# Kernel optimization log

Measured on AMD Instinct MI355X. Metric: run time of the kernel, lower is better.

## Reference

```python
import jax, jax.numpy as jnp
import numpy as np

SIG_EPS = 0.1
IN_DIM = 256
OUT_DIM = 64


def setup_inputs() -> dict:
    key = jax.random.key(0)
    ks = jax.random.split(key, 6)
    B, S, Q = 32, 512, 512
    return {
        "phi_support": jax.random.normal(ks[0], (B, S, IN_DIM), jnp.float32),
        "y_support": jax.random.normal(ks[1], (B, S, OUT_DIM), jnp.float32),
        "phi_query": jax.random.normal(ks[2], (B, Q, IN_DIM), jnp.float32),
        "y_query": jax.random.normal(ks[3], (B, Q, OUT_DIM), jnp.float32),
        # learned parameters (K init'd to zeros in torch, use small randn for a non-trivial test)
        "K": jax.random.normal(ks[4], (IN_DIM, OUT_DIM), jnp.float32) * 0.02,
        "L_asym": jax.random.normal(ks[5], (IN_DIM, IN_DIM), jnp.float32) * 0.1,
    }


def reference(phi_support, y_support, phi_query, y_query, K, L_asym):
    sig_eps = jnp.float32(SIG_EPS)
    log_sig_eps = jnp.log(sig_eps)
    out_dim = K.shape[1]

    L = L_asym @ L_asym.T  # [I, I]
    # nobs > 0 branch (n_support = 512)
    posterior_L = jnp.einsum('bsi,bsj->bij', phi_support, phi_support) + L[None]  # [B,I,I]
    posterior_L_inv = jnp.linalg.inv(posterior_L)
    rhs = jnp.einsum('bsi,bso->bio', phi_support, y_support) + (L @ K)[None]  # [B,I,O]
    posterior_K = posterior_L_inv @ rhs  # [B,I,O]

    mu_pred = phi_query @ posterior_K  # [B,Q,O]
    # spread_fac = 1 + diag quadratic form phi Linv phi^T  -> [B,Q]
    spread_fac = 1.0 + jnp.einsum('bqi,bij,bqj->bq', phi_query, posterior_L_inv, phi_query)
    eye_eps = jnp.eye(out_dim, dtype=phi_query.dtype) * sig_eps
    sig_pred = spread_fac[..., None, None] * eye_eps  # [B,Q,O,O]

    # predictive_nll: inverse of sig_pred is an exactly scaled identity, so the
    # quadratic form y^T inv(sig_pred) y == ||y||^2 / (spread_fac * sig_eps) (same math)
    diff = y_query - mu_pred
    quadf = jnp.sum(diff * diff, axis=-1) / (spread_fac * sig_eps)  # [B,Q]
    logdet = out_dim * (jnp.log(spread_fac) + log_sig_eps)  # [B,Q]
    predictive_nll = logdet.mean() + quadf.mean()

    return (mu_pred, sig_pred, predictive_nll)
```

## Files before the change

### kernel.cpp

```cpp
#include <hip/hip_runtime.h>
#include <hip/hip_cooperative_groups.h>
#include <math.h>

namespace cg = cooperative_groups;

#define B 32
#define S 512
#define Q 512
#define I 256
#define O 64
#define SIG_EPS 0.1f
#define LOG_SIG_EPS (-2.3025850929940457f)

#define WS_L 0
#define WS_T1 65536
#define WS_LKT 81920
#define WS_M0 98304
#define WS_M1 2195456
#define WS_RHST 4292608
#define WS_D 4816896
#define WS_U16 5079040
#define U_PTH 0
#define U_PTL 4194304
#define U_YTH 8388608
#define U_YTL 9437184
#define U_IVH 10485760
#define U_IVL 12582912
#define U_PKH 14680064
#define U_PKL 15204352

#define OUT_MU_ELEMS (B * Q * O)
#define OUT_SIG_ELEMS (B * Q * O * O)
#define OUT_NLL_IDX (OUT_MU_ELEMS + OUT_SIG_ELEMS)

typedef short short8 __attribute__((ext_vector_type(8)));
typedef float f32x4 __attribute__((ext_vector_type(4)));
#define MFMA16(a, b, c) __builtin_amdgcn_mfma_f32_16x16x32_bf16(a, b, c, 0, 0, 0)

struct Params {
  const float *phi_s, *y_s, *phi_q, *y_q, *Km, *La;
  float *Lm, *T1, *LKT, *M0, *M1, *RHST, *Dbuf;
  unsigned short *PTh, *PTl, *YTh, *YTl, *IVh, *IVl, *PKh, *PKl;
  float *mu, *nll;
  float4 *sig;
};

__device__ __forceinline__ f32x4 mfma3(short8 ah, short8 al, short8 bh, short8 bl, f32x4 c) {
  c = MFMA16(ah, bh, c);
  c = MFMA16(ah, bl, c);
  c = MFMA16(al, bh, c);
  return c;
}

__device__ __forceinline__ unsigned short f2bf(float x) {
  unsigned int u = __float_as_uint(x);
  return (unsigned short)((u + 0x7fffu + ((u >> 16) & 1u)) >> 16);
}
__device__ __forceinline__ float bf2f(unsigned short h) { return __uint_as_float(((unsigned int)h) << 16); }
__device__ __forceinline__ void split2(float x, unsigned short& h, unsigned short& l) {
  h = f2bf(x);
  l = f2bf(x - bf2f(h));
}
__device__ __forceinline__ void split4(float4 v, uint2& H, uint2& L) {
  unsigned short h0, h1, h2, h3, l0, l1, l2, l3;
  split2(v.x, h0, l0); split2(v.y, h1, l1); split2(v.z, h2, l2); split2(v.w, h3, l3);
  H.x = (unsigned)h0 | ((unsigned)h1 << 16); H.y = (unsigned)h2 | ((unsigned)h3 << 16);
  L.x = (unsigned)l0 | ((unsigned)l1 << 16); L.y = (unsigned)l2 | ((unsigned)l3 << 16);
}
__device__ __forceinline__ void cvt8(const float* p, short8& h8, short8& l8) {
  float4 a = *(const float4*)p;
  float4 b = *(const float4*)(p + 4);
  uint2 H0, L0, H1, L1;
  split4(a, H0, L0); split4(b, H1, L1);
  union { uint2 q[2]; short8 s; } uh, ul;
  uh.q[0] = H0; uh.q[1] = H1; ul.q[0] = L0; ul.q[1] = L1;
  h8 = uh.s; l8 = ul.s;
}
__device__ __forceinline__ short8 ld8(const unsigned short* p) { return *(const short8*)(const void*)p; }

__device__ __forceinline__ void fma4x4(const float4 av, const float4 bv, float acc[4][4]) {
  const float ar[4] = {av.x, av.y, av.z, av.w};
  const float br[4] = {bv.x, bv.y, bv.z, bv.w};
#pragma unroll
  for (int i = 0; i < 4; ++i)
#pragma unroll
    for (int j = 0; j < 4; ++j) acc[i][j] += ar[i] * br[j];
}

__device__ __forceinline__ void load_direct64(float* dst, int ds, const float* src, int ss, int t) {
#pragma unroll
  for (int m = 0; m < 4; ++m) {
    int r = (t >> 4) + 16 * m, c4 = (t & 15) * 4;
    *(float4*)&dst[r * ds + c4] = *(const float4*)&src[(size_t)r * ss + c4];
  }
}
__device__ __forceinline__ void load_trans64(float* dst, int ds, const float* src, int ss, int t) {
#pragma unroll
  for (int m = 0; m < 4; ++m) {
    int r = (t >> 4) + 16 * m, c4 = (t & 15) * 4;
    float4 v = *(const float4*)&src[(size_t)r * ss + c4];
    dst[(c4 + 0) * ds + r] = v.x;
    dst[(c4 + 1) * ds + r] = v.y;
    dst[(c4 + 2) * ds + r] = v.z;
    dst[(c4 + 3) * ds + r] = v.w;
  }
}
template <int SA, int SB>
__device__ __forceinline__ void gemm64(const float* At, const float* Bs, int tr, int tc, float acc[4][4]) {
#pragma unroll 8
  for (int kk = 0; kk < 64; ++kk) {
    float4 a = *(const float4*)&At[kk * SA + tr * 4];
    float4 b = *(const float4*)&Bs[kk * SB + tc * 4];
    fma4x4(a, b, acc);
  }
}

#define SC4(V) V.x *= pivinv; V.y *= pivinv; V.z *= pivinv; V.w *= pivinv
#define UP4(V, R) V.x -= g * R.x; V.y -= g * R.y; V.z -= g * R.z; V.w -= g * R.w

template <int TS>
__device__ void gj64(const float* T, float* rowbuf, float* Dout, int t) {
  int r = t >> 2, q = t & 3;
  int lane = t & 63;
  float4 A0 = *(const float4*)&T[r * TS + q * 16 + 0];
  float4 A1 = *(const float4*)&T[r * TS + q * 16 + 4];
  float4 A2 = *(const float4*)&T[r * TS + q * 16 + 8];
  float4 A3 = *(const float4*)&T[r * TS + q * 16 + 12];
#define IC(c) (((q * 16 + (c)) == r) ? 1.f : 0.f)
  float4 I0 = make_float4(IC(0), IC(1), IC(2), IC(3));
  float4 I1 = make_float4(IC(4), IC(5), IC(6), IC(7));
  float4 I2 = make_float4(IC(8), IC(9), IC(10), IC(11));
  float4 I3 = make_float4(IC(12), IC(13), IC(14), IC(15));
#undef IC
  for (int p = 0; p < 64; ++p) {
    float* RA = rowbuf + (p & 1) * 128;
    float* RI = RA + 64;
    if (r == p) {
      ((float4*)&RA[q * 16])[0] = A0; ((float4*)&RA[q * 16])[1] = A1;
      ((float4*)&RA[q * 16])[2] = A2; ((float4*)&RA[q * 16])[3] = A3;
      ((float4*)&RI[q * 16])[0] = I0; ((float4*)&RI[q * 16])[1] = I1;
      ((float4*)&RI[q * 16])[2] = I2; ((float4*)&RI[q * 16])[3] = I3;
    }
    __syncthreads();
    float pivinv = 1.0f / RA[p];
    int sidx = p & 15;
    float4 blk = (sidx < 8) ? ((sidx < 4) ? A0 : A1) : ((sidx < 12) ? A2 : A3);
    int sc = sidx & 3;
    float ap = (sc == 0) ? blk.x : (sc == 1) ? blk.y : (sc == 2) ? blk.z : blk.w;
    float f = __shfl(ap, (lane & ~3) | (p >> 4), 64);
    float4 ra0 = ((const float4*)&RA[q * 16])[0], ra1 = ((const float4*)&RA[q * 16])[1];
    float4 ra2 = ((const float4*)&RA[q * 16])[2], ra3 = ((const float4*)&RA[q * 16])[3];
    float4 ri0 = ((const float4*)&RI[q * 16])[0], ri1 = ((const float4*)&RI[q * 16])[1];
    float4 ri2 = ((const float4*)&RI[q * 16])[2], ri3 = ((const float4*)&RI[q * 16])[3];
    if (r == p) {
      SC4(A0); SC4(A1); SC4(A2); SC4(A3);
      SC4(I0); SC4(I1); SC4(I2); SC4(I3);
    } else {
      float g = f * pivinv;
      UP4(A0, ra0); UP4(A1, ra1); UP4(A2, ra2); UP4(A3, ra3);
      UP4(I0, ri0); UP4(I1, ri1); UP4(I2, ri2); UP4(I3, ri3);
    }
  }
  ((float4*)&Dout[r * 64 + q * 16])[0] = I0;
  ((float4*)&Dout[r * 64 + q * 16])[1] = I1;
  ((float4*)&Dout[r * 64 + q * 16])[2] = I2;
  ((float4*)&Dout[r * 64 + q * 16])[3] = I3;
}

__device__ void phase0_unit(const Params& p, int w, int t, float* smem) {
  if (w < 1280) {
    unsigned short* Hs = (unsigned short*)smem;
    unsigned short* Lo = Hs + 64 * 68;
    const float* src;
    unsigned short *dh, *dl;
    int sstride;
    if (w < 1024) {
      int b = w >> 5, r = w & 31, ic = r >> 3, sc = r & 7;
      src = p.phi_s + ((size_t)b * 512 + sc * 64) * 256 + ic * 64;
      sstride = 256;
      size_t d0 = ((size_t)b * 256 + ic * 64) * 512 + sc * 64;
      dh = p.PTh + d0; dl = p.PTl + d0;
    } else {
      int qq = w - 1024, b = qq >> 3, sc = qq & 7;
      src = p.y_s + ((size_t)b * 512 + sc * 64) * 64;
      sstride = 64;
      size_t d0 = ((size_t)b * 64) * 512 + sc * 64;
      dh = p.YTh + d0; dl = p.YTl + d0;
    }
    int c = t & 63, rb = (t >> 6) * 16;
#pragma unroll
    for (int m = 0; m < 16; ++m) {
      int s = rb + m;
      float x = src[(size_t)s * sstride + c];
      unsigned short h, l;
      split2(x, h, l);
      Hs[c * 68 + s] = h;
      Lo[c * 68 + s] = l;
    }
    __syncthreads();
    int il0 = t >> 4, c4 = (t & 15) * 4;
#pragma unroll
    for (int m = 0; m < 4; ++m) {
      int il = il0 + 16 * m;
      uint2 H, L;
      H.x = (unsigned)Hs[il * 68 + c4] | ((unsigned)Hs[il * 68 + c4 + 1] << 16);
      H.y = (unsigned)Hs[il * 68 + c4 + 2] | ((unsigned)Hs[il * 68 + c4 + 3] << 16);
      L.x = (unsigned)Lo[il * 68 + c4] | ((unsigned)Lo[il * 68 + c4 + 1] << 16);
      L.y = (unsigned)Lo[il * 68 + c4 + 2] | ((unsigned)Lo[il * 68 + c4 + 3] << 16);
      *(uint2*)&dh[(size_t)il * 512 + c4] = H;
      *(uint2*)&dl[(size_t)il * 512 + c4] = L;
    }
  } else {
    int blk2 = w - 1280;
    float* sA = smem;
    float* sB = smem + 1088;
    int tr = t >> 4, tc = t & 15;
    float acc[4][4] = {};
    if (blk2 < 16) {
      int i0 = (blk2 >> 2) * 64, j0 = (blk2 & 3) * 64;
      for (int ks = 0; ks < 256; ks += 16) {
        __syncthreads();
#pragma unroll
        for (int m = 0; m < 4; ++m) {
          int r = (t >> 4) + 16 * m, kk = t & 15;
          sA[kk * 68 + r] = p.La[(size_t)(i0 + r) * 256 + ks + kk];
          sB[kk * 68 + r] = p.La[(size_t)(j0 + r) * 256 + ks + kk];
        }
        __syncthreads();
#pragma unroll
        for (int kk = 0; kk < 16; ++kk) {
          float4 a = *(const float4*)&sA[kk * 68 + tr * 4];
          float4 bv = *(const float4*)&sB[kk * 68 + tc * 4];
          fma4x4(a, bv, acc);
        }
      }
#pragma unroll
      for (int mi = 0; mi < 4; ++mi) {
        float4 v = {acc[mi][0], acc[mi][1], acc[mi][2], acc[mi][3]};
        *(float4*)&p.Lm[(size_t)(i0 + tr * 4 + mi) * 256 + j0 + tc * 4] = v;
      }
    } else {
      int i0 = (blk2 - 16) * 64;
      for (int ks = 0; ks < 256; ks += 16) {
        __syncthreads();
#pragma unroll
        for (int m = 0; m < 4; ++m) {
          int kk = (t >> 6) + 4 * m, c = t & 63;
          sA[kk * 68 + c] = p.La[(size_t)(ks + kk) * 256 + i0 + c];
          sB[kk * 68 + c] = p.Km[(size_t)(ks + kk) * 64 + c];
        }
        __syncthreads();
#pragma unroll
        for (int kk = 0; kk < 16; ++kk) {
          float4 a = *(const float4*)&sA[kk * 68 + tr * 4];
          float4 bv = *(const float4*)&sB[kk * 68 + tc * 4];
          fma4x4(a, bv, acc);
        }
      }
#pragma unroll
      for (int mi = 0; mi < 4; ++mi) {
        float4 v = {acc[mi][0], acc[mi][1], acc[mi][2], acc[mi][3]};
        *(float4*)&p.T1[(size_t)(i0 + tr * 4 + mi) * 64 + tc * 4] = v;
      }
    }
  }
}

__device__ void gram_unit(const Params& p, int b, int u, int t, float* smem) {
  float* trbuf = smem;
  float* Ws = smem + 4352;
  float* rowb = smem + 12800;
  if (u == 15) return;
  if (u == 14) {
    if (b >= 4) return;
    int i0 = b * 64;
    int tr = t >> 4, tc = t & 15;
    float acc[4][4] = {};
    for (int ks = 0; ks < 256; ks += 16) {
      __syncthreads();
#pragma unroll
      for (int m = 0; m < 4; ++m) {
        trbuf[(t & 15) * 68 + (t >> 4) + 16 * m] = p.La[(size_t)(i0 + (t >> 4) + 16 * m) * 256 + ks + (t & 15)];
        Ws[((t >> 6) + 4 * m) * 64 + (t & 63)] = p.T1[(size_t)(ks + (t >> 6) + 4 * m) * 64 + (t & 63)];
      }
      __syncthreads();
#pragma unroll
      for (int kk = 0; kk < 16; ++kk) {
        float4 a = *(const float4*)&trbuf[kk * 68 + tr * 4];
        float4 bv = *(const float4*)&Ws[kk * 64 + tc * 4];
        fma4x4(a, bv, acc);
      }
    }
    __syncthreads();
#pragma unroll
    for (int mi = 0; mi < 4; ++mi)
#pragma unroll
      for (int cj = 0; cj < 4; ++cj) trbuf[(tr * 4 + mi) * 68 + tc * 4 + cj] = acc[mi][cj];
    __syncthreads();
    int rr0 = t >> 4, cc4 = (t & 15) * 4;
#pragma unroll
    for (int m = 0; m < 4; ++m) {
      int rr = rr0 + 16 * m;
      float4 v = {trbuf[(cc4 + 0) * 68 + rr], trbuf[(cc4 + 1) * 68 + rr], trbuf[(cc4 + 2) * 68 + rr],
                  trbuf[(cc4 + 3) * 68 + rr]};
      *(float4*)&p.LKT[(size_t)rr * 256 + i0 + cc4] = v;
    }
    return;
  }
  const int TIa[14] = {0, 0, 0, 0, 1, 1, 1, 2, 2, 3, 0, 1, 2, 3};
  const int TJa[14] = {0, 1, 2, 3, 1, 2, 3, 2, 3, 3, 0, 0, 0, 0};
  bool isR = (u >= 10);
  int it = TIa[u], jt = TJa[u];
  int i0 = it * 64, j0 = isR ? 0 : jt * 64;
  int lane = t & 63, w = t >> 6, wr = w >> 1, wc = w & 1;
  const unsigned short* Ah = p.PTh + (size_t)b * 256 * 512;
  const unsigned short* Al = p.PTl + (size_t)b * 256 * 512;
  const unsigned short* Bh = isR ? (p.YTh + (size_t)b * 64 * 512) : Ah;
  const unsigned short* Bl = isR ? (p.YTl + (size_t)b * 64 * 512) : Al;
  int ra0 = i0 + wr * 32 + (lane & 15);
  int rb0 = j0 + wc * 32 + (lane & 15);
  int klane = (lane >> 4) * 8;
  f32x4 acc[2][2] = {};
  for (int ks = 0; ks < 512; ks += 32) {
    int kk = ks + klane;
    short8 a0h = ld8(Ah + (size_t)ra0 * 512 + kk);
    short8 a1h = ld8(Ah + (size_t)(ra0 + 16) * 512 + kk);
    short8 a0l = ld8(Al + (size_t)ra0 * 512 + kk);
    short8 a1l = ld8(Al + (size_t)(ra0 + 16) * 512 + kk);
    short8 b0h = ld8(Bh + (size_t)rb0 * 512 + kk);
    short8 b1h = ld8(Bh + (size_t)(rb0 + 16) * 512 + kk);
    short8 b0l = ld8(Bl + (size_t)rb0 * 512 + kk);
    short8 b1l = ld8(Bl + (size_t)(rb0 + 16) * 512 + kk);
    acc[0][0] = mfma3(a0h, a0l, b0h, b0l, acc[0][0]);
    acc[0][1] = mfma3(a0h, a0l, b1h, b1l, acc[0][1]);
    acc[1][0] = mfma3(a1h, a1l, b0h, b0l, acc[1][0]);
    acc[1][1] = mfma3(a1h, a1l, b1h, b1l, acc[1][1]);
  }
#pragma unroll
  for (int ti = 0; ti < 2; ++ti)
#pragma unroll
    for (int tj = 0; tj < 2; ++tj)
#pragma unroll
      for (int r = 0; r < 4; ++r)
        trbuf[(wr * 32 + ti * 16 + (lane >> 4) * 4 + r) * 68 + wc * 32 + tj * 16 + (lane & 15)] = acc[ti][tj][r];
  __syncthreads();
  int rr0 = t >> 4, cc4 = (t & 15) * 4;
  if (!isR) {
    float* Mb = p.M0 + (size_t)b * 65536;
    bool d00 = (it == 0 && jt == 0);
#pragma unroll
    for (int m = 0; m < 4; ++m) {
      int rr = rr0 + 16 * m;
      float4 v = *(float4*)&trbuf[rr * 68 + cc4];
      float4 lv = *(const float4*)&p.Lm[(size_t)(i0 + rr) * 256 + j0 + cc4];
      v.x += lv.x; v.y += lv.y; v.z += lv.z; v.w += lv.w;
      *(float4*)&Mb[(size_t)(i0 + rr) * 256 + j0 + cc4] = v;
      if (d00) *(float4*)&trbuf[rr * 68 + cc4] = v;
    }
    if (it != jt) {
#pragma unroll
      for (int m = 0; m < 4; ++m) {
        int rr = rr0 + 16 * m;
        float4 v = {trbuf[(cc4 + 0) * 68 + rr], trbuf[(cc4 + 1) * 68 + rr], trbuf[(cc4 + 2) * 68 + rr],
                    trbuf[(cc4 + 3) * 68 + rr]};
        float4 lv = *(const float4*)&p.Lm[(size_t)(j0 + rr) * 256 + i0 + cc4];
        v.x += lv.x; v.y += lv.y; v.z += lv.z; v.w += lv.w;
        *(float4*)&Mb[(size_t)(j0 + rr) * 256 + i0 + cc4] = v;
      }
    }
    if (d00) {
      __syncthreads();
      gj64<68>(trbuf, rowb, p.Dbuf + (size_t)b * 4096, t);
    }
  } else {
#pragma unroll
    for (int m = 0; m < 4; ++m) {
      int rr = rr0 + 16 * m;
      float4 v = {trbuf[(cc4 + 0) * 68 + rr], trbuf[(cc4 + 1) * 68 + rr], trbuf[(cc4 + 2) * 68 + rr],
                  trbuf[(cc4 + 3) * 68 + rr]};
      *(float4*)&p.RHST[((size_t)b * 64 + rr) * 256 + i0 + cc4] = v;
    }
  }
}

__device__ void st_unit(const Params& p, int b, int u, int kb, int t, float* smem) {
  float* shA = smem;
  float* shB = smem + 4352;
  float* shD = smem + 8448;
  float* rowb = smem + 12800;
  int i = u >> 2, j = u & 3;
  int tr = t >> 4, tc = t & 15;
  const float* Ms = ((kb & 1) ? p.M1 : p.M0) + (size_t)b * 65536;
  float* Md = ((kb & 1) ? p.M0 : p.M1) + (size_t)b * 65536;
  const float* Din = p.Dbuf + (size_t)(kb & 1) * (B * 4096) + (size_t)b * 4096;
  float* Dout = p.Dbuf + (size_t)((kb + 1) & 1) * (B * 4096) + (size_t)b * 4096;
  bool last = (kb == 3);
  unsigned short* Yh = p.IVh + (size_t)b * 65536;
  unsigned short* Yl = p.IVl + (size_t)b * 65536;
  auto STORE = [&](int row, int col, float4 v) {
    if (last) {
      uint2 H, L;
      split4(v, H, L);
      *(uint2*)&Yh[(size_t)row * 256 + col] = H;
      *(uint2*)&Yl[(size_t)row * 256 + col] = L;
    } else {
      *(float4*)&Md[(size_t)row * 256 + col] = v;
    }
  };
  bool ik = (i == kb), jk = (j == kb);
  if (ik && jk) {
#pragma unroll
    for (int m = 0; m < 4; ++m) {
      int r = (t >> 4) + 16 * m, c4 = (t & 15) * 4;
      STORE(kb * 64 + r, kb * 64 + c4, *(const float4*)&Din[r * 64 + c4]);
    }
  } else if (ik) {
    float acc[4][4] = {};
    load_trans64(shA, 68, Din, 64, t);
    load_direct64(shB, 64, &Ms[(size_t)(kb * 64) * 256 + j * 64], 256, t);
    __syncthreads();
    gemm64<68, 64>(shA, shB, tr, tc, acc);
    __syncthreads();
#pragma unroll
    for (int mi = 0; mi < 4; ++mi) {
      float4 v = {acc[mi][0], acc[mi][1], acc[mi][2], acc[mi][3]};
      STORE(kb * 64 + tr * 4 + mi, j * 64 + tc * 4, v);
    }
  } else if (jk) {
    float acc[4][4] = {};
    load_trans64(shA, 68, &Ms[(size_t)(i * 64) * 256 + kb * 64], 256, t);
    load_direct64(shB, 64, Din, 64, t);
    __syncthreads();
    gemm64<68, 64>(shA, shB, tr, tc, acc);
    __syncthreads();
#pragma unroll
    for (int mi = 0; mi < 4; ++mi) {
      float4 v = {-acc[mi][0], -acc[mi][1], -acc[mi][2], -acc[mi][3]};
      STORE(i * 64 + tr * 4 + mi, kb * 64 + tc * 4, v);
    }
  } else {
    float acc[4][4] = {};
    load_trans64(shA, 68, Din, 64, t);
    load_direct64(shB, 64, &Ms[(size_t)(kb * 64) * 256 + j * 64], 256, t);
    load_trans64(shD, 68, &Ms[(size_t)(i * 64) * 256 + kb * 64], 256, t);
    __syncthreads();
    gemm64<68, 64>(shA, shB, tr, tc, acc);
    __syncthreads();
#pragma unroll
    for (int mi = 0; mi < 4; ++mi) {
      float4 v = {acc[mi][0], acc[mi][1], acc[mi][2], acc[mi][3]};
      *(float4*)&shB[(tr * 4 + mi) * 64 + tc * 4] = v;
    }
    __syncthreads();
    float acc2[4][4] = {};
    gemm64<68, 64>(shD, shB, tr, tc, acc2);
    bool la = (kb < 3) && (i == kb + 1) && (j == kb + 1);
    if (la) __syncthreads();
#pragma unroll
    for (int mi = 0; mi < 4; ++mi) {
      size_t off = (size_t)(i * 64 + tr * 4 + mi) * 256 + j * 64 + tc * 4;
      float4 old = *(const float4*)&Ms[off];
      float4 v = {old.x - acc2[mi][0], old.y - acc2[mi][1], old.z - acc2[mi][2], old.w - acc2[mi][3]};
      STORE(i * 64 + tr * 4 + mi, j * 64 + tc * 4, v);
      if (la) *(float4*)&shB[(tr * 4 + mi) * 64 + tc * 4] = v;
    }
    if (la) {
      __syncthreads();
      gj64<64>(shB, rowb, Dout, t);
    }
  }
}

__device__ void postk_unit(const Params& p, int b, int u, int t) {
  int i0 = u * 64;
  int lane = t & 63, w = t >> 6, wr = w >> 1, wc = w & 1;
  const unsigned short* Ah = p.IVh + (size_t)b * 65536;
  const unsigned short* Al = p.IVl + (size_t)b * 65536;
  int ra0 = i0 + wr * 32 + (lane & 15);
  int ob0 = wc * 32 + (lane & 15);
  int klane = (lane >> 4) * 8;
  f32x4 acc[2][2] = {};
  for (int ks = 0; ks < 256; ks += 32) {
    int kk = ks + klane;
    short8 a0h = ld8(Ah + (size_t)ra0 * 256 + kk);
    short8 a1h = ld8(Ah + (size_t)(ra0 + 16) * 256 + kk);
    short8 a0l = ld8(Al + (size_t)ra0 * 256 + kk);
    short8 a1l = ld8(Al + (size_t)(ra0 + 16) * 256 + kk);
    short8 bh[2], bl[2];
#pragma unroll
    for (int sjj = 0; sjj < 2; ++sjj) {
      int o = ob0 + sjj * 16;
      float g[8];
      float4 g0 = *(const float4*)&p.RHST[((size_t)b * 64 + o) * 256 + kk];
      float4 g1 = *(const float4*)&p.RHST[((size_t)b * 64 + o) * 256 + kk + 4];
      float4 l0 = *(const float4*)&p.LKT[(size_t)o * 256 + kk];
      float4 l1 = *(const float4*)&p.LKT[(size_t)o * 256 + kk + 4];
      g[0] = g0.x + l0.x; g[1] = g0.y + l0.y; g[2] = g0.z + l0.z; g[3] = g0.w + l0.w;
      g[4] = g1.x + l1.x; g[5] = g1.y + l1.y; g[6] = g1.z + l1.z; g[7] = g1.w + l1.w;
      cvt8(g, bh[sjj], bl[sjj]);
    }
    acc[0][0] = mfma3(a0h, a0l, bh[0], bl[0], acc[0][0]);
    acc[0][1] = mfma3(a0h, a0l, bh[1], bl[1], acc[0][1]);
    acc[1][0] = mfma3(a1h, a1l, bh[0], bl[0], acc[1][0]);
    acc[1][1] = mfma3(a1h, a1l, bh[1], bl[1], acc[1][1]);
  }
#pragma unroll
  for (int ti = 0; ti < 2; ++ti)
#pragma unroll
    for (int tj = 0; tj < 2; ++tj) {
      int ib = i0 + wr * 32 + ti * 16 + (lane >> 4) * 4;
      int o = wc * 32 + tj * 16 + (lane & 15);
      float4 v = {acc[ti][tj][0], acc[ti][tj][1], acc[ti][tj][2], acc[ti][tj][3]};
      uint2 H, L;
      split4(v, H, L);
      *(uint2*)&p.PKh[((size_t)b * 64 + o) * 256 + ib] = H;
      *(uint2*)&p.PKl[((size_t)b * 64 + o) * 256 + ib] = L;
    }
}

__device__ void tail_unit(const Params& p, int b, int qb, int t, float* smem) {
  float (*red)[4] = (float(*)[4])smem;
  float* spf = smem + 128;
  int lane = t & 63, w = t >> 6;
  int hs = w >> 1;
  int s = w & 1;
  int rows16 = qb + hs * 16;
  int qlane = rows16 + (lane & 15);
  int klane = (lane >> 4) * 8;
  const float* Pq = p.phi_q + (size_t)b * 512 * 256;
  short8 ah[8], al[8];
#pragma unroll
  for (int k8 = 0; k8 < 8; ++k8) cvt8(&Pq[(size_t)qlane * 256 + k8 * 32 + klane], ah[k8], al[k8]);

  const unsigned short* Kh = p.PKh + (size_t)b * 16384;
  const unsigned short* Kl = p.PKl + (size_t)b * 16384;
  float ssdr[4] = {0.f, 0.f, 0.f, 0.f};
#pragma unroll
  for (int oi = 0; oi < 2; ++oi) {
    int ot = s * 2 + oi;
    f32x4 acc = {};
    int orow = ot * 16 + (lane & 15);
#pragma unroll
    for (int k8 = 0; k8 < 8; ++k8) {
      short8 bh = ld8(Kh + (size_t)orow * 256 + k8 * 32 + klane);
      short8 bl = ld8(Kl + (size_t)orow * 256 + k8 * 32 + klane);
      acc = mfma3(ah[k8], al[k8], bh, bl, acc);
    }
#pragma unroll
    for (int r = 0; r < 4; ++r) {
      int qrow = rows16 + (lane >> 4) * 4 + r;
      int o = ot * 16 + (lane & 15);
      float m = acc[r];
      p.mu[((size_t)b * 512 + qrow) * 64 + o] = m;
      float d = p.y_q[((size_t)b * 512 + qrow) * 64 + o] - m;
      ssdr[r] += d * d;
    }
  }
  const unsigned short* Vh = p.IVh + (size_t)b * 65536;
  const unsigned short* Vl = p.IVl + (size_t)b * 65536;
  float rs[4] = {0.f, 0.f, 0.f, 0.f};
  for (int jt = s * 8; jt < s * 8 + 8; ++jt) {
    f32x4 acc = {};
    int jrow = jt * 16 + (lane & 15);
#pragma unroll
    for (int k8 = 0; k8 < 8; ++k8) {
      short8 bh = ld8(Vh + (size_t)jrow * 256 + k8 * 32 + klane);
      short8 bl = ld8(Vl + (size_t)jrow * 256 + k8 * 32 + klane);
      acc = mfma3(ah[k8], al[k8], bh, bl, acc);
    }
#pragma unroll
    for (int r = 0; r < 4; ++r) {
      int qrow = rows16 + (lane >> 4) * 4 + r;
      rs[r] += acc[r] * Pq[(size_t)qrow * 256 + jt * 16 + (lane & 15)];
    }
  }
#pragma unroll
  for (int off = 1; off < 16; off <<= 1)
#pragma unroll
    for (int r = 0; r < 4; ++r) {
      rs[r] += __shfl_xor(rs[r], off);
      ssdr[r] += __shfl_xor(ssdr[r], off);
    }
  if ((lane & 15) == 0) {
#pragma unroll
    for (int r = 0; r < 4; ++r) {
      int rloc = hs * 16 + (lane >> 4) * 4 + r;
      red[rloc][s] = rs[r];
      red[rloc][2 + s] = ssdr[r];
    }
  }
  __syncthreads();
  if (w == 0) {
    float val = 0.f;
    if (t < 32) {
      float sp = 1.f + red[t][0] + red[t][1];
      spf[t] = sp;
      float ssd = red[t][2] + red[t][3];
      val = (64.f * (logf(sp) + LOG_SIG_EPS) + ssd / (sp * SIG_EPS)) * (1.0f / 16384.0f);
    }
#pragma unroll
    for (int off = 32; off; off >>= 1) val += __shfl_down(val, off);
    if (t == 0) atomicAdd(p.nll, val);
  }
  __syncthreads();
  size_t base = ((size_t)b * 512 + qb) * 1024;
#pragma unroll 4
  for (int it = 0; it < 128; ++it) {
    int idx = it * 256 + t;
    int rloc = idx >> 10;
    int o = (idx >> 4) & 63;
    int p4 = idx & 15;
    float sv = spf[rloc] * SIG_EPS;
    float4 v;
    v.x = (p4 * 4 + 0 == o) ? sv : 0.f;
    v.y = (p4 * 4 + 1 == o) ? sv : 0.f;
    v.z = (p4 * 4 + 2 == o) ? sv : 0.f;
    v.w = (p4 * 4 + 3 == o) ? sv : 0.f;
    p.sig[base + idx] = v;
  }
}

__global__ __launch_bounds__(256) void k_all(Params p) {
  cg::grid_group grid = cg::this_grid();
  __shared__ float smem[13056];
  int g = blockIdx.x, t = threadIdx.x;
  if (g == 0 && t == 0) p.nll[0] = 0.f;
  for (int w = g; w < 1300; w += 256) {
    __syncthreads();
    phase0_unit(p, w, t, smem);
  }
  __threadfence();
  grid.sync();
  for (int w = g; w < 512; w += 256) {
    __syncthreads();
    gram_unit(p, w >> 4, w & 15, t, smem);
  }
  __threadfence();
  grid.sync();
  for (int kb = 0; kb < 4; ++kb) {
    for (int w = g; w < 512; w += 256) {
      __syncthreads();
      st_unit(p, w >> 4, w & 15, kb, t, smem);
    }
    __threadfence();
    grid.sync();
  }
  for (int w = g; w < 128; w += 256) postk_unit(p, w >> 2, w & 3, t);
  __threadfence();
  grid.sync();
  for (int w = g; w < 512; w += 256) {
    __syncthreads();
    tail_unit(p, w >> 4, (w & 15) * 32, t, smem);
  }
}

__global__ __launch_bounds__(256) void k_p0(Params p) {
  __shared__ float smem[13056];
  if (blockIdx.x == 0 && threadIdx.x == 0) p.nll[0] = 0.f;
  phase0_unit(p, blockIdx.x, threadIdx.x, smem);
}
__global__ __launch_bounds__(256) void k_gramw(Params p) {
  __shared__ float smem[13056];
  gram_unit(p, blockIdx.x >> 4, blockIdx.x & 15, threadIdx.x, smem);
}
__global__ __launch_bounds__(256) void k_stw(Params p, int kb) {
  __shared__ float smem[13056];
  st_unit(p, blockIdx.x >> 4, blockIdx.x & 15, kb, threadIdx.x, smem);
}
__global__ __launch_bounds__(256) void k_postkw(Params p) {
  postk_unit(p, blockIdx.x >> 2, blockIdx.x & 3, threadIdx.x);
}
__global__ __launch_bounds__(256) void k_tailw(Params p) {
  __shared__ float smem[13056];
  tail_unit(p, blockIdx.x >> 4, (blockIdx.x & 15) * 32, threadIdx.x, smem);
}

extern "C" void kernel_launch(void* const* d_in, const int* in_sizes, int n_in, void* d_out, int out_size,
                              void* d_ws, size_t ws_size, hipStream_t stream) {
  float* ws = (float*)d_ws;
  unsigned short* u16b = (unsigned short*)(ws + WS_U16);
  float* out_mu = (float*)d_out;

  Params p;
  p.phi_s = (const float*)d_in[0];
  p.y_s = (const float*)d_in[1];
  p.phi_q = (const float*)d_in[2];
  p.y_q = (const float*)d_in[3];
  p.Km = (const float*)d_in[4];
  p.La = (const float*)d_in[5];
  p.Lm = ws + WS_L;
  p.T1 = ws + WS_T1;
  p.LKT = ws + WS_LKT;
  p.M0 = ws + WS_M0;
  p.M1 = ws + WS_M1;
  p.RHST = ws + WS_RHST;
  p.Dbuf = ws + WS_D;
  p.PTh = u16b + U_PTH;
  p.PTl = u16b + U_PTL;
  p.YTh = u16b + U_YTH;
  p.YTl = u16b + U_YTL;
  p.IVh = u16b + U_IVH;
  p.IVl = u16b + U_IVL;
  p.PKh = u16b + U_PKH;
  p.PKl = u16b + U_PKL;
  p.mu = out_mu;
  p.sig = (float4*)(out_mu + OUT_MU_ELEMS);
  p.nll = out_mu + OUT_NLL_IDX;

  int dev = 0;
  hipGetDevice(&dev);
  int coop = 0;
  hipDeviceGetAttribute(&coop, hipDeviceAttributeCooperativeLaunch, dev);
  int maxb = 0;
  hipOccupancyMaxActiveBlocksPerMultiprocessor(&maxb, (const void*)k_all, 256, 0);

  if (coop && maxb >= 1) {
    void* kargs[1] = {(void*)&p};
    hipLaunchCooperativeKernel((const void*)k_all, dim3(256, 1, 1), dim3(256, 1, 1), kargs, 0, stream);
  } else {
    k_p0<<<1300, 256, 0, stream>>>(p);
    k_gramw<<<512, 256, 0, stream>>>(p);
    for (int kb = 0; kb < 4; ++kb) k_stw<<<512, 256, 0, stream>>>(p, kb);
    k_postkw<<<128, 256, 0, stream>>>(p);
    k_tailw<<<512, 256, 0, stream>>>(p);
  }
}
```

Measured before the change: 351.6 us.

## Replace cooperative grid-sync kernel with per-stage launches and reassociate mu computation

Drops the single cooperative kernel with grid.sync barriers and launches separate kernels per stage, each sized to its work with smaller per-kernel shared memory. The posterior-K GEMM stage is removed. mu is now computed as (phi_q·Linv)·rhs, reusing the phi_q·Linv product already needed for the spread factor and keeping it in LDS. The RHS+LK bias add moves into an extra block row of the first elimination step. This trades grid-wide barriers for kernel launch gaps, and the mu product becomes a plain fp32 FMA loop in place of split-bf16 MFMA.

```diff
diff --git a/kernel.cpp b/kernel.cpp
--- a/kernel.cpp
+++ b/kernel.cpp
@@ -1,8 +1,5 @@
 #include <hip/hip_runtime.h>
-#include <hip/hip_cooperative_groups.h>
 #include <math.h>
-
-namespace cg = cooperative_groups;
 
 #define B 32
 #define S 512
@@ -26,8 +23,6 @@
 #define U_YTL 9437184
 #define U_IVH 10485760
 #define U_IVL 12582912
-#define U_PKH 14680064
-#define U_PKL 15204352
 
 #define OUT_MU_ELEMS (B * Q * O)
 #define OUT_SIG_ELEMS (B * Q * O * O)
@@ -40,7 +35,7 @@
 struct Params {
   const float *phi_s, *y_s, *phi_q, *y_q, *Km, *La;
   float *Lm, *T1, *LKT, *M0, *M1, *RHST, *Dbuf;
-  unsigned short *PTh, *PTl, *YTh, *YTl, *IVh, *IVl, *PKh, *PKl;
+  unsigned short *PTh, *PTl, *YTh, *YTl, *IVh, *IVl;
   float *mu, *nll;
   float4 *sig;
 };
@@ -167,7 +162,10 @@
   ((float4*)&Dout[r * 64 + q * 16])[3] = I3;
 }
 
-__device__ void phase0_unit(const Params& p, int w, int t, float* smem) {
+__global__ __launch_bounds__(256) void k_front(Params p) {
+  __shared__ float smem[4352];
+  int w = blockIdx.x, t = threadIdx.x;
+  if (w == 0 && t == 0) p.nll[0] = 0.f;
   if (w < 1280) {
     unsigned short* Hs = (unsigned short*)smem;
     unsigned short* Lo = Hs + 64 * 68;
@@ -266,11 +264,12 @@
   }
 }
 
-__device__ void gram_unit(const Params& p, int b, int u, int t, float* smem) {
+__global__ __launch_bounds__(256) void k_gram(Params p) {
+  __shared__ float smem[5632];
   float* trbuf = smem;
   float* Ws = smem + 4352;
-  float* rowb = smem + 12800;
-  if (u == 15) return;
+  float* rowb = smem + 5376;
+  int b = blockIdx.x, u = blockIdx.y, t = threadIdx.x;
   if (u == 14) {
     if (b >= 4) return;
     int i0 = b * 64;
@@ -383,11 +382,26 @@
   }
 }
 
-__device__ void st_unit(const Params& p, int b, int u, int kb, int t, float* smem) {
+__global__ __launch_bounds__(256) void k_st(Params p, int kb) {
+  __shared__ float smem[13056];
   float* shA = smem;
   float* shB = smem + 4352;
   float* shD = smem + 8448;
   float* rowb = smem + 12800;
+  int b = blockIdx.x, u = blockIdx.y, t = threadIdx.x;
+  if (u == 16) {
+    float4* R4 = (float4*)(p.RHST + (size_t)b * 16384);
+    const float4* L4 = (const float4*)p.LKT;
+#pragma unroll
+    for (int m = 0; m < 16; ++m) {
+      int idx = m * 256 + t;
+      float4 a = R4[idx];
+      float4 l = L4[idx];
+      a.x += l.x; a.y += l.y; a.z += l.z; a.w += l.w;
+      R4[idx] = a;
+    }
+    return;
+  }
   int i = u >> 2, j = u & 3;
   int tr = t >> 4, tc = t & 15;
   const float* Ms = ((kb & 1) ? p.M1 : p.M0) + (size_t)b * 65536;
@@ -471,56 +485,12 @@
   }
 }
 
-__device__ void postk_unit(const Params& p, int b, int u, int t) {
-  int i0 = u * 64;
-  int lane = t & 63, w = t >> 6, wr = w >> 1, wc = w & 1;
-  const unsigned short* Ah = p.IVh + (size_t)b * 65536;
-  const unsigned short* Al = p.IVl + (size_t)b * 65536;
-  int ra0 = i0 + wr * 32 + (lane & 15);
-  int ob0 = wc * 32 + (lane & 15);
-  int klane = (lane >> 4) * 8;
-  f32x4 acc[2][2] = {};
-  for (int ks = 0; ks < 256; ks += 32) {
-    int kk = ks + klane;
-    short8 a0h = ld8(Ah + (size_t)ra0 * 256 + kk);
-    short8 a1h = ld8(Ah + (size_t)(ra0 + 16) * 256 + kk);
-    short8 a0l = ld8(Al + (size_t)ra0 * 256 + kk);
-    short8 a1l = ld8(Al + (size_t)(ra0 + 16) * 256 + kk);
-    short8 bh[2], bl[2];
-#pragma unroll
-    for (int sjj = 0; sjj < 2; ++sjj) {
-      int o = ob0 + sjj * 16;
-      float g[8];
-      float4 g0 = *(const float4*)&p.RHST[((size_t)b * 64 + o) * 256 + kk];
-      float4 g1 = *(const float4*)&p.RHST[((size_t)b * 64 + o) * 256 + kk + 4];
-      float4 l0 = *(const float4*)&p.LKT[(size_t)o * 256 + kk];
-      float4 l1 = *(const float4*)&p.LKT[(size_t)o * 256 + kk + 4];
-      g[0] = g0.x + l0.x; g[1] = g0.y + l0.y; g[2] = g0.z + l0.z; g[3] = g0.w + l0.w;
-      g[4] = g1.x + l1.x; g[5] = g1.y + l1.y; g[6] = g1.z + l1.z; g[7] = g1.w + l1.w;
-      cvt8(g, bh[sjj], bl[sjj]);
-    }
-    acc[0][0] = mfma3(a0h, a0l, bh[0], bl[0], acc[0][0]);
-    acc[0][1] = mfma3(a0h, a0l, bh[1], bl[1], acc[0][1]);
-    acc[1][0] = mfma3(a1h, a1l, bh[0], bl[0], acc[1][0]);
-    acc[1][1] = mfma3(a1h, a1l, bh[1], bl[1], acc[1][1]);
-  }
-#pragma unroll
-  for (int ti = 0; ti < 2; ++ti)
-#pragma unroll
-    for (int tj = 0; tj < 2; ++tj) {
-      int ib = i0 + wr * 32 + ti * 16 + (lane >> 4) * 4;
-      int o = wc * 32 + tj * 16 + (lane & 15);
-      float4 v = {acc[ti][tj][0], acc[ti][tj][1], acc[ti][tj][2], acc[ti][tj][3]};
-      uint2 H, L;
-      split4(v, H, L);
-      *(uint2*)&p.PKh[((size_t)b * 64 + o) * 256 + ib] = H;
-      *(uint2*)&p.PKl[((size_t)b * 64 + o) * 256 + ib] = L;
-    }
-}
-
-__device__ void tail_unit(const Params& p, int b, int qb, int t, float* smem) {
-  float (*red)[4] = (float(*)[4])smem;
-  float* spf = smem + 128;
+__global__ __launch_bounds__(256) void k_tail(Params p) {
+  __shared__ float Xlds[32 * 264];
+  __shared__ float red[32][2];
+  __shared__ float spf[32];
+  __shared__ float ssdl[32];
+  int b = blockIdx.x, qb = blockIdx.y * 32, t = threadIdx.x;
   int lane = t & 63, w = t >> 6;
   int hs = w >> 1;
   int s = w & 1;
@@ -532,30 +502,6 @@
 #pragma unroll
   for (int k8 = 0; k8 < 8; ++k8) cvt8(&Pq[(size_t)qlane * 256 + k8 * 32 + klane], ah[k8], al[k8]);
 
-  const unsigned short* Kh = p.PKh + (size_t)b * 16384;
-  const unsigned short* Kl = p.PKl + (size_t)b * 16384;
-  float ssdr[4] = {0.f, 0.f, 0.f, 0.f};
-#pragma unroll
-  for (int oi = 0; oi < 2; ++oi) {
-    int ot = s * 2 + oi;
-    f32x4 acc = {};
-    int orow = ot * 16 + (lane & 15);
-#pragma unroll
-    for (int k8 = 0; k8 < 8; ++k8) {
-      short8 bh = ld8(Kh + (size_t)orow * 256 + k8 * 32 + klane);
-      short8 bl = ld8(Kl + (size_t)orow * 256 + k8 * 32 + klane);
-      acc = mfma3(ah[k8], al[k8], bh, bl, acc);
-    }
-#pragma unroll
-    for (int r = 0; r < 4; ++r) {
-      int qrow = rows16 + (lane >> 4) * 4 + r;
-      int o = ot * 16 + (lane & 15);
-      float m = acc[r];
-      p.mu[((size_t)b * 512 + qrow) * 64 + o] = m;
-      float d = p.y_q[((size_t)b * 512 + qrow) * 64 + o] - m;
-      ssdr[r] += d * d;
-    }
-  }
   const unsigned short* Vh = p.IVh + (size_t)b * 65536;
   const unsigned short* Vl = p.IVl + (size_t)b * 65536;
   float rs[4] = {0.f, 0.f, 0.f, 0.f};
@@ -570,39 +516,72 @@
     }
 #pragma unroll
     for (int r = 0; r < 4; ++r) {
-      int qrow = rows16 + (lane >> 4) * 4 + r;
-      rs[r] += acc[r] * Pq[(size_t)qrow * 256 + jt * 16 + (lane & 15)];
+      int xq = hs * 16 + (lane >> 4) * 4 + r;
+      int xi = jt * 16 + (lane & 15);
+      Xlds[xq * 264 + xi] = acc[r];
+      rs[r] += acc[r] * Pq[(size_t)(rows16 + (lane >> 4) * 4 + r) * 256 + xi];
     }
   }
 #pragma unroll
   for (int off = 1; off < 16; off <<= 1)
 #pragma unroll
-    for (int r = 0; r < 4; ++r) {
-      rs[r] += __shfl_xor(rs[r], off);
-      ssdr[r] += __shfl_xor(ssdr[r], off);
-    }
+    for (int r = 0; r < 4; ++r) rs[r] += __shfl_xor(rs[r], off);
   if ((lane & 15) == 0) {
 #pragma unroll
-    for (int r = 0; r < 4; ++r) {
-      int rloc = hs * 16 + (lane >> 4) * 4 + r;
-      red[rloc][s] = rs[r];
-      red[rloc][2 + s] = ssdr[r];
-    }
+    for (int r = 0; r < 4; ++r) red[hs * 16 + (lane >> 4) * 4 + r][s] = rs[r];
   }
   __syncthreads();
+
+  if (t < 32) spf[t] = 1.f + red[t][0] + red[t][1];
+
+  {
+    int q = t >> 3, o0 = (t & 7) * 8;
+    const float* Gr = p.RHST + (size_t)b * 16384;
+    float accv[8] = {};
+#pragma unroll 2
+    for (int i = 0; i < 256; i += 4) {
+      float4 xv = *(const float4*)&Xlds[q * 264 + i];
+#pragma unroll
+      for (int oo = 0; oo < 8; ++oo) {
+        float4 gv = *(const float4*)&Gr[(size_t)(o0 + oo) * 256 + i];
+        accv[oo] += xv.x * gv.x + xv.y * gv.y + xv.z * gv.z + xv.w * gv.w;
+      }
+    }
+    size_t qg = (size_t)b * 512 + qb + q;
+    float4 m0 = {accv[0], accv[1], accv[2], accv[3]};
+    float4 m1 = {accv[4], accv[5], accv[6], accv[7]};
+    *(float4*)&p.mu[qg * 64 + o0] = m0;
+    *(float4*)&p.mu[qg * 64 + o0 + 4] = m1;
+    float4 y0 = *(const float4*)&p.y_q[qg * 64 + o0];
+    float4 y1 = *(const float4*)&p.y_q[qg * 64 + o0 + 4];
+    float d;
+    float ssd8 = 0.f;
+    d = y0.x - m0.x; ssd8 += d * d;
+    d = y0.y - m0.y; ssd8 += d * d;
+    d = y0.z - m0.z; ssd8 += d * d;
+    d = y0.w - m0.w; ssd8 += d * d;
+    d = y1.x - m1.x; ssd8 += d * d;
+    d = y1.y - m1.y; ssd8 += d * d;
+    d = y1.z - m1.z; ssd8 += d * d;
+    d = y1.w - m1.w; ssd8 += d * d;
+    ssd8 += __shfl_xor(ssd8, 1);
+    ssd8 += __shfl_xor(ssd8, 2);
+    ssd8 += __shfl_xor(ssd8, 4);
+    if ((t & 7) == 0) ssdl[q] = ssd8;
+  }
+  __syncthreads();
+
   if (w == 0) {
     float val = 0.f;
     if (t < 32) {
-      float sp = 1.f + red[t][0] + red[t][1];
-      spf[t] = sp;
-      float ssd = red[t][2] + red[t][3];
-      val = (64.f * (logf(sp) + LOG_SIG_EPS) + ssd / (sp * SIG_EPS)) * (1.0f / 16384.0f);
+      float sp = spf[t];
+      val = (64.f * (logf(sp) + LOG_SIG_EPS) + ssdl[t] / (sp * SIG_EPS)) * (1.0f / 16384.0f);
     }
 #pragma unroll
     for (int off = 32; off; off >>= 1) val += __shfl_down(val, off);
     if (t == 0) atomicAdd(p.nll, val);
   }
-  __syncthreads();
+
   size_t base = ((size_t)b * 512 + qb) * 1024;
 #pragma unroll 4
   for (int it = 0; it < 128; ++it) {
@@ -618,61 +597,6 @@
     v.w = (p4 * 4 + 3 == o) ? sv : 0.f;
     p.sig[base + idx] = v;
   }
-}
-
-__global__ __launch_bounds__(256) void k_all(Params p) {
-  cg::grid_group grid = cg::this_grid();
-  __shared__ float smem[13056];
-  int g = blockIdx.x, t = threadIdx.x;
-  if (g == 0 && t == 0) p.nll[0] = 0.f;
-  for (int w = g; w < 1300; w += 256) {
-    __syncthreads();
-    phase0_unit(p, w, t, smem);
-  }
-  __threadfence();
-  grid.sync();
-  for (int w = g; w < 512; w += 256) {
-    __syncthreads();
-    gram_unit(p, w >> 4, w & 15, t, smem);
-  }
-  __threadfence();
-  grid.sync();
-  for (int kb = 0; kb < 4; ++kb) {
-    for (int w = g; w < 512; w += 256) {
-      __syncthreads();
-      st_unit(p, w >> 4, w & 15, kb, t, smem);
-    }
-    __threadfence();
-    grid.sync();
-  }
-  for (int w = g; w < 128; w += 256) postk_unit(p, w >> 2, w & 3, t);
-  __threadfence();
-  grid.sync();
-  for (int w = g; w < 512; w += 256) {
-    __syncthreads();
-    tail_unit(p, w >> 4, (w & 15) * 32, t, smem);
-  }
-}
-
-__global__ __launch_bounds__(256) void k_p0(Params p) {
-  __shared__ float smem[13056];
-  if (blockIdx.x == 0 && threadIdx.x == 0) p.nll[0] = 0.f;
-  phase0_unit(p, blockIdx.x, threadIdx.x, smem);
-}
-__global__ __launch_bounds__(256) void k_gramw(Params p) {
-  __shared__ float smem[13056];
-  gram_unit(p, blockIdx.x >> 4, blockIdx.x & 15, threadIdx.x, smem);
-}
-__global__ __launch_bounds__(256) void k_stw(Params p, int kb) {
-  __shared__ float smem[13056];
-  st_unit(p, blockIdx.x >> 4, blockIdx.x & 15, kb, threadIdx.x, smem);
-}
-__global__ __launch_bounds__(256) void k_postkw(Params p) {
-  postk_unit(p, blockIdx.x >> 2, blockIdx.x & 3, threadIdx.x);
-}
-__global__ __launch_bounds__(256) void k_tailw(Params p) {
-  __shared__ float smem[13056];
-  tail_unit(p, blockIdx.x >> 4, (blockIdx.x & 15) * 32, threadIdx.x, smem);
 }
 
 extern "C" void kernel_launch(void* const* d_in, const int* in_sizes, int n_in, void* d_out, int out_size,
@@ -701,27 +625,15 @@
   p.YTl = u16b + U_YTL;
   p.IVh = u16b + U_IVH;
   p.IVl = u16b + U_IVL;
-  p.PKh = u16b + U_PKH;
-  p.PKl = u16b + U_PKL;
   p.mu = out_mu;
   p.sig = (float4*)(out_mu + OUT_MU_ELEMS);
   p.nll = out_mu + OUT_NLL_IDX;
 
-  int dev = 0;
-  hipGetDevice(&dev);
-  int coop = 0;
-  hipDeviceGetAttribute(&coop, hipDeviceAttributeCooperativeLaunch, dev);
-  int maxb = 0;
-  hipOccupancyMaxActiveBlocksPerMultiprocessor(&maxb, (const void*)k_all, 256, 0);
-
-  if (coop && maxb >= 1) {
-    void* kargs[1] = {(void*)&p};
-    hipLaunchCooperativeKernel((const void*)k_all, dim3(256, 1, 1), dim3(256, 1, 1), kargs, 0, stream);
-  } else {
-    k_p0<<<1300, 256, 0, stream>>>(p);
-    k_gramw<<<512, 256, 0, stream>>>(p);
-    for (int kb = 0; kb < 4; ++kb) k_stw<<<512, 256, 0, stream>>>(p, kb);
-    k_postkw<<<128, 256, 0, stream>>>(p);
-    k_tailw<<<512, 256, 0, stream>>>(p);
-  }
-}
+  k_front<<<1300, 256, 0, stream>>>(p);
+  k_gram<<<dim3(B, 15), 256, 0, stream>>>(p);
+  k_st<<<dim3(B, 17), 256, 0, stream>>>(p, 0);
+  k_st<<<dim3(B, 16), 256, 0, stream>>>(p, 1);
+  k_st<<<dim3(B, 16), 256, 0, stream>>>(p, 2);
+  k_st<<<dim3(B, 16), 256, 0, stream>>>(p, 3);
+  k_tail<<<dim3(B, 16), 256, 0, stream>>>(p);
+}
```

Result: slower. 416.6 us (+18.5%).
